# Performance work log

Hardware: AMD Instinct MI355X
Metric: run time of the kernel (lower is better)

## Reference

```python
import jax, jax.numpy as jnp
import numpy as np

ALPHA = 1.5
BETA = 0.5
AVG_RATIO = 1.0
SUM_TIMESTEPS = 28000
RANK = 8
K_TOP = RANK * RANK  # k = weight_1_a.shape[1] * weight_2_a.shape[1]


def setup_inputs() -> dict:
    key = jax.random.key(0)
    ks = jax.random.split(key, 5)
    B, S, D_IN, D_OUT = 2, 4096, 4096, 4096
    return {
        "hidden_states": jax.random.normal(ks[0], (B, S, D_IN), dtype=jnp.float32),
        "weight_1_a": jax.random.normal(ks[1], (D_OUT, RANK), dtype=jnp.float32) * 0.02,
        "weight_1_b": jax.random.normal(ks[2], (RANK, D_IN), dtype=jnp.float32) * 0.02,
        "weight_2_a": jax.random.normal(ks[3], (D_OUT, RANK), dtype=jnp.float32) * 0.02,
        "weight_2_b": jax.random.normal(ks[4], (RANK, D_IN), dtype=jnp.float32) * 0.02,
        "timestep": 1,
    }


def reference(hidden_states, weight_1_a, weight_1_b, weight_2_a, weight_2_b, timestep):
    # Low-rank expansions: [out, rank] @ [rank, in] -> [out, in]
    matrix1 = weight_1_a @ weight_1_b
    matrix2 = weight_2_a @ weight_2_b
    top_k_sum1 = jax.lax.top_k(jnp.abs(matrix1).ravel(), K_TOP)[0].sum()
    top_k_sum2 = jax.lax.top_k(jnp.abs(matrix2).ravel(), K_TOP)[0].sum()
    time_ratio = timestep % SUM_TIMESTEPS
    scale = (ALPHA * time_ratio / SUM_TIMESTEPS + BETA) % ALPHA  # pattern 's*'
    temp_ratio = (top_k_sum1 / AVG_RATIO) / (top_k_sum2 * scale)
    weight = jnp.where(temp_ratio > 1.0, matrix1, matrix2)  # [out, in]
    # F.linear: x @ W^T
    return jnp.einsum("bsi,oi->bso", hidden_states, weight)
```

## Files before the change

kernel.cpp:

```cpp
#include <hip/hip_runtime.h>
#include <stdint.h>

#define D 4096
#define RANK 8
#define ALPHA 1.5f
#define BETA 0.5f
#define SUM_TIMESTEPS 28000
#define K_TOP 64
#define NBINS 1024

typedef float f32x4 __attribute__((ext_vector_type(4)));

#define WS_HCNT_OFF 256
#define WS_HSUM_OFF (256 + 2 * NBINS * 4)
#define WS_ZERO_WORDS 6208

#define FIX_NUM 2.74877906944e11f
#define FIX_INV 3.637978807091713e-12

__global__ __launch_bounds__(1024) void k_init(unsigned* __restrict__ w) {
    for (int i = threadIdx.x; i < WS_ZERO_WORDS; i += 1024) w[i] = 0u;
}

__device__ __forceinline__ float dot4v(f32x4 a, f32x4 b) {
    return fmaf(a.x, b.x, fmaf(a.y, b.y, fmaf(a.z, b.z, a.w * b.w)));
}

__global__ __launch_bounds__(256) void k_pass_max(
    const float* __restrict__ wa1, const float* __restrict__ wb1,
    const float* __restrict__ wa2, const float* __restrict__ wb2,
    unsigned* __restrict__ hdr) {
    const int tid = threadIdx.x;
    const int mat = blockIdx.y;
    const float* __restrict__ wa = mat ? wa2 : wa1;
    const float* __restrict__ wb = mat ? wb2 : wb1;
    const int i0 = (blockIdx.x & 3) * 1024 + tid * 4;
    const int obase = (blockIdx.x >> 2) * 64;

    f32x4 wbv[RANK];
#pragma unroll
    for (int r = 0; r < RANK; ++r)
        wbv[r] = *(const f32x4*)(wb + r * D + i0);

    float vmax = 0.f;
#pragma unroll 4
    for (int oo = 0; oo < 64; ++oo) {
        const float* __restrict__ war = wa + (size_t)(obase + oo) * RANK;
        f32x4 s = {0.f, 0.f, 0.f, 0.f};
#pragma unroll
        for (int r = 0; r < RANK; ++r) {
            const float a = war[r];
            s.x = fmaf(a, wbv[r].x, s.x);
            s.y = fmaf(a, wbv[r].y, s.y);
            s.z = fmaf(a, wbv[r].z, s.z);
            s.w = fmaf(a, wbv[r].w, s.w);
        }
        vmax = fmaxf(vmax, fmaxf(fmaxf(fabsf(s.x), fabsf(s.y)),
                                 fmaxf(fabsf(s.z), fabsf(s.w))));
    }
    for (int off = 32; off; off >>= 1)
        vmax = fmaxf(vmax, __shfl_xor(vmax, off, 64));
    __shared__ float smax[4];
    const int wave = tid >> 6, lane = tid & 63;
    if (lane == 0) smax[wave] = vmax;
    __syncthreads();
    if (tid == 0) {
        float m = fmaxf(fmaxf(smax[0], smax[1]), fmaxf(smax[2], smax[3]));
        atomicMax(&hdr[mat], __float_as_uint(m));
    }
}

__global__ __launch_bounds__(256) void k_pass_hist(
    const float* __restrict__ wa1, const float* __restrict__ wb1,
    const float* __restrict__ wa2, const float* __restrict__ wb2,
    const unsigned* __restrict__ hdr,
    unsigned* __restrict__ gcnt, unsigned long long* __restrict__ gsum) {
    __shared__ unsigned lcnt[NBINS];
    __shared__ unsigned long long lsum[NBINS];
    const int tid = threadIdx.x;
    const int mat = blockIdx.y;
    for (int b = tid; b < NBINS; b += 256) { lcnt[b] = 0u; lsum[b] = 0ull; }
    __syncthreads();

    const float* __restrict__ wa = mat ? wa2 : wa1;
    const float* __restrict__ wb = mat ? wb2 : wb1;
    const float M = __uint_as_float(hdr[mat]);
    const float T = 0.5f * M;
    const float fix = FIX_NUM / M;
    const unsigned bitsT = __float_as_uint(T);
    const int i0 = (blockIdx.x & 3) * 1024 + tid * 4;
    const int obase = (blockIdx.x >> 2) * 64;

    f32x4 wbv[RANK];
#pragma unroll
    for (int r = 0; r < RANK; ++r)
        wbv[r] = *(const f32x4*)(wb + r * D + i0);

#pragma unroll 2
    for (int oo = 0; oo < 64; ++oo) {
        const float* __restrict__ war = wa + (size_t)(obase + oo) * RANK;
        f32x4 s = {0.f, 0.f, 0.f, 0.f};
#pragma unroll
        for (int r = 0; r < RANK; ++r) {
            const float a = war[r];
            s.x = fmaf(a, wbv[r].x, s.x);
            s.y = fmaf(a, wbv[r].y, s.y);
            s.z = fmaf(a, wbv[r].z, s.z);
            s.w = fmaf(a, wbv[r].w, s.w);
        }
        const float av[4] = {fabsf(s.x), fabsf(s.y), fabsf(s.z), fabsf(s.w)};
#pragma unroll
        for (int j = 0; j < 4; ++j) {
            if (av[j] >= T) {
                unsigned k = (__float_as_uint(av[j]) - bitsT) >> 13;
                if (k > NBINS - 1u) k = NBINS - 1u;
                atomicAdd(&lcnt[k], 1u);
                atomicAdd(&lsum[k], (unsigned long long)(av[j] * fix));
            }
        }
    }
    __syncthreads();
    unsigned* __restrict__ gc = gcnt + (size_t)mat * NBINS;
    unsigned long long* __restrict__ gs = gsum + (size_t)mat * NBINS;
    for (int b = tid; b < NBINS; b += 256) {
        unsigned c = lcnt[b];
        if (c) {
            atomicAdd(&gc[b], c);
            atomicAdd(&gs[b], lsum[b]);
        }
    }
}

__global__ __launch_bounds__(1024) void k_select(
    unsigned* __restrict__ hdr,
    const unsigned* __restrict__ gcnt, const unsigned long long* __restrict__ gsum,
    const int* __restrict__ tsp) {
    __shared__ unsigned sc[NBINS];
    __shared__ unsigned long long ss[NBINS];
    __shared__ float res[2];
    __shared__ int sB;
    const int b = threadIdx.x;

    for (int mat = 0; mat < 2; ++mat) {
        if (b == 0) sB = -1;
        const unsigned c0 = gcnt[(size_t)mat * NBINS + b];
        const unsigned long long s0 = gsum[(size_t)mat * NBINS + b];
        __syncthreads();
        sc[b] = c0;
        ss[b] = s0;
        __syncthreads();
        for (int step = 1; step < NBINS; step <<= 1) {
            unsigned c2 = 0u; unsigned long long s2 = 0ull;
            if (b + step < NBINS) { c2 = sc[b + step]; s2 = ss[b + step]; }
            __syncthreads();
            sc[b] += c2;
            ss[b] += s2;
            __syncthreads();
        }
        if (sc[b] >= K_TOP && (b == NBINS - 1 || sc[b + 1] < K_TOP)) sB = b;
        __syncthreads();
        if (b == 0) {
            const float M = __uint_as_float(hdr[mat]);
            const double inv = (double)M * FIX_INV;
            float total;
            if (sB < 0) {
                total = (float)((double)ss[0] * inv);
            } else {
                const int B = sB;
                const unsigned cAbove = (B + 1 < NBINS) ? sc[B + 1] : 0u;
                const unsigned long long sAbove = (B + 1 < NBINS) ? ss[B + 1] : 0ull;
                const unsigned cb = sc[B] - cAbove;
                const unsigned long long sb = ss[B] - sAbove;
                const unsigned need = K_TOP - cAbove;
                total = (float)((double)sAbove * inv)
                      + (float)((double)sb * inv) * ((float)need / (float)cb);
            }
            res[mat] = total;
        }
        __syncthreads();
    }
    if (b == 0) {
        const int tr = (*tsp) % SUM_TIMESTEPS;
        const float scale = fmodf(ALPHA * (float)tr / (float)SUM_TIMESTEPS + BETA, ALPHA);
        const float temp_ratio = res[0] / (res[1] * scale);
        hdr[4] = (temp_ratio > 1.0f) ? 1u : 0u;
    }
}

__global__ __launch_bounds__(512) void k_fused(
    const float* __restrict__ h,
    const float* __restrict__ wa1, const float* __restrict__ wb1,
    const float* __restrict__ wa2, const float* __restrict__ wb2,
    const unsigned* __restrict__ hdr,
    float* __restrict__ out) {
    const int tid = threadIdx.x;
    const int wave = tid >> 6, lane = tid & 63;
    const unsigned flag = hdr[4];
    const float* __restrict__ wa = flag ? wa1 : wa2;
    const float* __restrict__ wb = flag ? wb1 : wb2;
    const size_t m0 = (size_t)blockIdx.x * 16;
    const int r0 = wave * 2;

    __shared__ float wbs[RANK][2048];
    __shared__ float ts[16][8];

    float acc[2][RANK];
#pragma unroll
    for (int row = 0; row < 2; ++row)
#pragma unroll
        for (int r = 0; r < RANK; ++r) acc[row][r] = 0.f;

    for (int hh = 0; hh < 2; ++hh) {
        __syncthreads();
        {
            const f32x4* __restrict__ src = (const f32x4*)wb;
            f32x4* __restrict__ dst = (f32x4*)wbs;
#pragma unroll
            for (int q = 0; q < 8; ++q) {
                const int j = q * 512 + tid;
                const int r = j >> 9;
                const int c4 = j & 511;
                dst[j] = src[r * 1024 + hh * 512 + c4];
            }
        }
        __syncthreads();
#pragma unroll 4
        for (int k = 0; k < 8; ++k) {
            const int il = k * 256 + lane * 4;
            f32x4 wbv[RANK];
#pragma unroll
            for (int r = 0; r < RANK; ++r)
                wbv[r] = *(const f32x4*)&wbs[r][il];
            f32x4 hv[2];
#pragma unroll
            for (int row = 0; row < 2; ++row)
                hv[row] = *(const f32x4*)(h + (m0 + r0 + row) * D + hh * 2048 + il);
#pragma unroll
            for (int row = 0; row < 2; ++row)
#pragma unroll
                for (int r = 0; r < RANK; ++r)
                    acc[row][r] = fmaf(hv[row].x, wbv[r].x,
                                  fmaf(hv[row].y, wbv[r].y,
                                  fmaf(hv[row].z, wbv[r].z,
                                  fmaf(hv[row].w, wbv[r].w, acc[row][r]))));
        }
    }

#pragma unroll
    for (int row = 0; row < 2; ++row)
#pragma unroll
        for (int r = 0; r < RANK; ++r)
#pragma unroll
            for (int off = 32; off; off >>= 1)
                acc[row][r] += __shfl_xor(acc[row][r], off, 64);
    if (lane == 0) {
#pragma unroll
        for (int row = 0; row < 2; ++row)
#pragma unroll
            for (int r = 0; r < RANK; ++r)
                ts[r0 + row][r] = acc[row][r];
    }
    __syncthreads();

#pragma unroll
    for (int cc = 0; cc < 2; ++cc) {
        const int o0 = wave * 512 + cc * 256 + lane * 4;
        f32x4 A[8];
#pragma unroll
        for (int j = 0; j < 8; ++j)
            A[j] = *(const f32x4*)(wa + (size_t)o0 * RANK + j * 4);
#pragma unroll 4
        for (int row = 0; row < 16; ++row) {
            const f32x4 t03 = *(const f32x4*)&ts[row][0];
            const f32x4 t47 = *(const f32x4*)&ts[row][4];
            f32x4 ov;
            ov.x = dot4v(A[0], t03) + dot4v(A[1], t47);
            ov.y = dot4v(A[2], t03) + dot4v(A[3], t47);
            ov.z = dot4v(A[4], t03) + dot4v(A[5], t47);
            ov.w = dot4v(A[6], t03) + dot4v(A[7], t47);
            __builtin_nontemporal_store(ov, (f32x4*)(out + (m0 + row) * D + o0));
        }
    }
}

extern "C" void kernel_launch(void* const* d_in, const int* in_sizes, int n_in,
                              void* d_out, int out_size, void* d_ws, size_t ws_size,
                              hipStream_t stream) {
    const float* h   = (const float*)d_in[0];
    const float* wa1 = (const float*)d_in[1];
    const float* wb1 = (const float*)d_in[2];
    const float* wa2 = (const float*)d_in[3];
    const float* wb2 = (const float*)d_in[4];
    const int*   ts  = (const int*)d_in[5];
    float* out = (float*)d_out;

    const int rows = in_sizes[0] / D;

    unsigned* hdr  = (unsigned*)d_ws;
    unsigned* gcnt = (unsigned*)((char*)d_ws + WS_HCNT_OFF);
    unsigned long long* gsum = (unsigned long long*)((char*)d_ws + WS_HSUM_OFF);

    hipLaunchKernelGGL(k_init, dim3(1), dim3(1024), 0, stream, (unsigned*)d_ws);
    hipLaunchKernelGGL(k_pass_max, dim3(256, 2), dim3(256), 0, stream,
                       wa1, wb1, wa2, wb2, hdr);
    hipLaunchKernelGGL(k_pass_hist, dim3(256, 2), dim3(256), 0, stream,
                       wa1, wb1, wa2, wb2, hdr, gcnt, gsum);
    hipLaunchKernelGGL(k_select, dim3(1), dim3(1024), 0, stream,
                       hdr, gcnt, gsum, ts);
    hipLaunchKernelGGL(k_fused, dim3(rows / 16), dim3(512), 0, stream,
                       h, wa1, wb1, wa2, wb2, hdr, out);
}
```

Measured before the change: 105.5 us.

## Drop init kernel via per-block max partials and retile fused kernel to 256 threads

Removes the separate workspace-zeroing kernel. k_pass_max now zeroes the histogram counters itself and writes per-block maxima instead of using a global atomicMax, and the hist and select kernels reduce those 256 partials locally. The fused projection kernel moves to 256 threads with 4 rows per wave, staging wb in four quarter chunks so the LDS footprint is halved. This saves one launch and the atomics but adds redundant max reductions in every hist block, and the larger register tile may change occupancy.

```diff
diff --git a/kernel.cpp b/kernel.cpp
--- a/kernel.cpp
+++ b/kernel.cpp
@@ -11,16 +11,12 @@
 
 typedef float f32x4 __attribute__((ext_vector_type(4)));
 
-#define WS_HCNT_OFF 256
-#define WS_HSUM_OFF (256 + 2 * NBINS * 4)
-#define WS_ZERO_WORDS 6208
+#define WS_GCNT_OFF 256
+#define WS_GSUM_OFF (256 + 2 * NBINS * 4)
+#define WS_BMAX_OFF (WS_GSUM_OFF + 2 * NBINS * 8)
 
 #define FIX_NUM 2.74877906944e11f
 #define FIX_INV 3.637978807091713e-12
-
-__global__ __launch_bounds__(1024) void k_init(unsigned* __restrict__ w) {
-    for (int i = threadIdx.x; i < WS_ZERO_WORDS; i += 1024) w[i] = 0u;
-}
 
 __device__ __forceinline__ float dot4v(f32x4 a, f32x4 b) {
     return fmaf(a.x, b.x, fmaf(a.y, b.y, fmaf(a.z, b.z, a.w * b.w)));
@@ -29,13 +25,16 @@
 __global__ __launch_bounds__(256) void k_pass_max(
     const float* __restrict__ wa1, const float* __restrict__ wb1,
     const float* __restrict__ wa2, const float* __restrict__ wb2,
-    unsigned* __restrict__ hdr) {
+    unsigned* __restrict__ gz, unsigned* __restrict__ bmax) {
     const int tid = threadIdx.x;
     const int mat = blockIdx.y;
+    const int bid = blockIdx.x;
+    if (mat == 0 && tid < 24) gz[bid * 24 + tid] = 0u;
+
     const float* __restrict__ wa = mat ? wa2 : wa1;
     const float* __restrict__ wb = mat ? wb2 : wb1;
-    const int i0 = (blockIdx.x & 3) * 1024 + tid * 4;
-    const int obase = (blockIdx.x >> 2) * 64;
+    const int i0 = (bid & 3) * 1024 + tid * 4;
+    const int obase = (bid >> 2) * 64;
 
     f32x4 wbv[RANK];
 #pragma unroll
@@ -66,25 +65,37 @@
     __syncthreads();
     if (tid == 0) {
         float m = fmaxf(fmaxf(smax[0], smax[1]), fmaxf(smax[2], smax[3]));
-        atomicMax(&hdr[mat], __float_as_uint(m));
-    }
+        bmax[mat * 256 + bid] = __float_as_uint(m);
+    }
+}
+
+__device__ __forceinline__ float block_max256(const unsigned* __restrict__ bmax,
+                                              int mat, int tid, float* redm) {
+    const int wave = tid >> 6, lane = tid & 63;
+    float m = 0.f;
+    if (tid < 256) m = __uint_as_float(bmax[mat * 256 + tid]);
+    for (int off = 32; off; off >>= 1)
+        m = fmaxf(m, __shfl_xor(m, off, 64));
+    if (tid < 256 && lane == 0) redm[wave] = m;
+    __syncthreads();
+    return fmaxf(fmaxf(redm[0], redm[1]), fmaxf(redm[2], redm[3]));
 }
 
 __global__ __launch_bounds__(256) void k_pass_hist(
     const float* __restrict__ wa1, const float* __restrict__ wb1,
     const float* __restrict__ wa2, const float* __restrict__ wb2,
-    const unsigned* __restrict__ hdr,
+    const unsigned* __restrict__ bmax,
     unsigned* __restrict__ gcnt, unsigned long long* __restrict__ gsum) {
     __shared__ unsigned lcnt[NBINS];
     __shared__ unsigned long long lsum[NBINS];
+    __shared__ float redm[4];
     const int tid = threadIdx.x;
     const int mat = blockIdx.y;
     for (int b = tid; b < NBINS; b += 256) { lcnt[b] = 0u; lsum[b] = 0ull; }
-    __syncthreads();
+    const float M = block_max256(bmax, mat, tid, redm);
 
     const float* __restrict__ wa = mat ? wa2 : wa1;
     const float* __restrict__ wb = mat ? wb2 : wb1;
-    const float M = __uint_as_float(hdr[mat]);
     const float T = 0.5f * M;
     const float fix = FIX_NUM / M;
     const unsigned bitsT = __float_as_uint(T);
@@ -132,14 +143,22 @@
 }
 
 __global__ __launch_bounds__(1024) void k_select(
-    unsigned* __restrict__ hdr,
+    unsigned* __restrict__ hdr, const unsigned* __restrict__ bmax,
     const unsigned* __restrict__ gcnt, const unsigned long long* __restrict__ gsum,
     const int* __restrict__ tsp) {
     __shared__ unsigned sc[NBINS];
     __shared__ unsigned long long ss[NBINS];
     __shared__ float res[2];
+    __shared__ float Ms[2];
+    __shared__ float redm[4];
     __shared__ int sB;
     const int b = threadIdx.x;
+
+    for (int mat = 0; mat < 2; ++mat) {
+        float M = block_max256(bmax, mat, b, redm);
+        if (b == 0) Ms[mat] = M;
+        __syncthreads();
+    }
 
     for (int mat = 0; mat < 2; ++mat) {
         if (b == 0) sB = -1;
@@ -160,8 +179,7 @@
         if (sc[b] >= K_TOP && (b == NBINS - 1 || sc[b + 1] < K_TOP)) sB = b;
         __syncthreads();
         if (b == 0) {
-            const float M = __uint_as_float(hdr[mat]);
-            const double inv = (double)M * FIX_INV;
+            const double inv = (double)Ms[mat] * FIX_INV;
             float total;
             if (sB < 0) {
                 total = (float)((double)ss[0] * inv);
@@ -187,7 +205,7 @@
     }
 }
 
-__global__ __launch_bounds__(512) void k_fused(
+__global__ __launch_bounds__(256) void k_fused(
     const float* __restrict__ h,
     const float* __restrict__ wa1, const float* __restrict__ wb1,
     const float* __restrict__ wa2, const float* __restrict__ wb2,
@@ -199,44 +217,44 @@
     const float* __restrict__ wa = flag ? wa1 : wa2;
     const float* __restrict__ wb = flag ? wb1 : wb2;
     const size_t m0 = (size_t)blockIdx.x * 16;
-    const int r0 = wave * 2;
-
-    __shared__ float wbs[RANK][2048];
+    const int r0w = wave * 4;
+
+    __shared__ float wbs[RANK][1024];
     __shared__ float ts[16][8];
 
-    float acc[2][RANK];
-#pragma unroll
-    for (int row = 0; row < 2; ++row)
+    float acc[4][RANK];
+#pragma unroll
+    for (int row = 0; row < 4; ++row)
 #pragma unroll
         for (int r = 0; r < RANK; ++r) acc[row][r] = 0.f;
 
-    for (int hh = 0; hh < 2; ++hh) {
+    for (int q = 0; q < 4; ++q) {
         __syncthreads();
         {
             const f32x4* __restrict__ src = (const f32x4*)wb;
             f32x4* __restrict__ dst = (f32x4*)wbs;
 #pragma unroll
-            for (int q = 0; q < 8; ++q) {
-                const int j = q * 512 + tid;
-                const int r = j >> 9;
-                const int c4 = j & 511;
-                dst[j] = src[r * 1024 + hh * 512 + c4];
+            for (int t = 0; t < 8; ++t) {
+                const int j = t * 256 + tid;
+                const int r = j >> 8;
+                const int c = j & 255;
+                dst[j] = src[r * 1024 + q * 256 + c];
             }
         }
         __syncthreads();
-#pragma unroll 4
-        for (int k = 0; k < 8; ++k) {
+#pragma unroll
+        for (int k = 0; k < 4; ++k) {
             const int il = k * 256 + lane * 4;
             f32x4 wbv[RANK];
 #pragma unroll
             for (int r = 0; r < RANK; ++r)
                 wbv[r] = *(const f32x4*)&wbs[r][il];
-            f32x4 hv[2];
-#pragma unroll
-            for (int row = 0; row < 2; ++row)
-                hv[row] = *(const f32x4*)(h + (m0 + r0 + row) * D + hh * 2048 + il);
-#pragma unroll
-            for (int row = 0; row < 2; ++row)
+            f32x4 hv[4];
+#pragma unroll
+            for (int row = 0; row < 4; ++row)
+                hv[row] = *(const f32x4*)(h + (m0 + r0w + row) * D + q * 1024 + il);
+#pragma unroll
+            for (int row = 0; row < 4; ++row)
 #pragma unroll
                 for (int r = 0; r < RANK; ++r)
                     acc[row][r] = fmaf(hv[row].x, wbv[r].x,
@@ -247,7 +265,7 @@
     }
 
 #pragma unroll
-    for (int row = 0; row < 2; ++row)
+    for (int row = 0; row < 4; ++row)
 #pragma unroll
         for (int r = 0; r < RANK; ++r)
 #pragma unroll
@@ -255,16 +273,16 @@
                 acc[row][r] += __shfl_xor(acc[row][r], off, 64);
     if (lane == 0) {
 #pragma unroll
-        for (int row = 0; row < 2; ++row)
+        for (int row = 0; row < 4; ++row)
 #pragma unroll
             for (int r = 0; r < RANK; ++r)
-                ts[r0 + row][r] = acc[row][r];
+                ts[r0w + row][r] = acc[row][r];
     }
     __syncthreads();
 
 #pragma unroll
-    for (int cc = 0; cc < 2; ++cc) {
-        const int o0 = wave * 512 + cc * 256 + lane * 4;
+    for (int cc = 0; cc < 4; ++cc) {
+        const int o0 = wave * 1024 + cc * 256 + lane * 4;
         f32x4 A[8];
 #pragma unroll
         for (int j = 0; j < 8; ++j)
@@ -297,16 +315,16 @@
     const int rows = in_sizes[0] / D;
 
     unsigned* hdr  = (unsigned*)d_ws;
-    unsigned* gcnt = (unsigned*)((char*)d_ws + WS_HCNT_OFF);
-    unsigned long long* gsum = (unsigned long long*)((char*)d_ws + WS_HSUM_OFF);
-
-    hipLaunchKernelGGL(k_init, dim3(1), dim3(1024), 0, stream, (unsigned*)d_ws);
+    unsigned* gcnt = (unsigned*)((char*)d_ws + WS_GCNT_OFF);
+    unsigned long long* gsum = (unsigned long long*)((char*)d_ws + WS_GSUM_OFF);
+    unsigned* bmax = (unsigned*)((char*)d_ws + WS_BMAX_OFF);
+
     hipLaunchKernelGGL(k_pass_max, dim3(256, 2), dim3(256), 0, stream,
-                       wa1, wb1, wa2, wb2, hdr);
+                       wa1, wb1, wa2, wb2, gcnt, bmax);
     hipLaunchKernelGGL(k_pass_hist, dim3(256, 2), dim3(256), 0, stream,
-                       wa1, wb1, wa2, wb2, hdr, gcnt, gsum);
+                       wa1, wb1, wa2, wb2, bmax, gcnt, gsum);
     hipLaunchKernelGGL(k_select, dim3(1), dim3(1024), 0, stream,
-                       hdr, gcnt, gsum, ts);
-    hipLaunchKernelGGL(k_fused, dim3(rows / 16), dim3(512), 0, stream,
+                       hdr, bmax, gcnt, gsum, ts);
+    hipLaunchKernelGGL(k_fused, dim3(rows / 16), dim3(256), 0, stream,
                        h, wa1, wb1, wa2, wb2, hdr, out);
 }
```

After: 107.4 us. No clear change (+1.8%).
